# Performance work log

Measured on AMD Instinct MI355X. Metric: run time of the kernel, lower is better.

## Reference

```python
import jax, jax.numpy as jnp
import numpy as np

LAMBDA = 0.5
TAU = 1.0
EPS = 1e-8  # torch F.cosine_similarity eps

B, D = 8192, 1024


def setup_inputs() -> dict:
    key = jax.random.key(0)
    k1, k2, k3, k4 = jax.random.split(key, 4)
    return {
        "student_query_emb": jax.random.normal(k1, (B, D), dtype=jnp.float32),
        "student_passage_emb": jax.random.normal(k2, (B, D), dtype=jnp.float32),
        "teacher_query_emb": jax.random.normal(k3, (B, D), dtype=jnp.float32),
        "teacher_passage_emb": jax.random.normal(k4, (B, D), dtype=jnp.float32),
    }


def _mse(a, b):
    d = a - b
    return jnp.mean(d * d)


def _retrieval_loss(q, p):
    # cosine sim = (q . p) / max(||q|| * ||p||, eps); normalize then matmul
    # (avoids the [B,B,D] broadcast intermediate of the torch version)
    qn = q / jnp.maximum(jnp.linalg.norm(q, axis=-1, keepdims=True), EPS)
    pn = p / jnp.maximum(jnp.linalg.norm(p, axis=-1, keepdims=True), EPS)
    logits = jnp.einsum("bd,cd->bc", qn, pn) / TAU  # [B, B]
    # cross-entropy with labels = arange(B): pick the diagonal log-prob
    logprobs = jax.nn.log_softmax(logits, axis=-1)
    return -jnp.mean(jnp.diagonal(logprobs))


def reference(student_query_emb, student_passage_emb, teacher_query_emb, teacher_passage_emb):
    distill = 0.5 * (_mse(student_query_emb, teacher_query_emb)
                     + _mse(student_passage_emb, teacher_passage_emb))
    retrieval = _retrieval_loss(student_query_emb, student_passage_emb)
    return LAMBDA * distill + (1.0 - LAMBDA) * retrieval
```

## Files before the change

kernel.cpp:

```cpp
#include <hip/hip_runtime.h>
#include <hip/hip_bf16.h>

typedef unsigned short u16;
typedef unsigned char u8;
typedef float f32x4 __attribute__((ext_vector_type(4)));
typedef int int4v __attribute__((ext_vector_type(4)));
typedef int int8v __attribute__((ext_vector_type(8)));

#define B_ROWS 8192
#define D_DIM  1024
#define FP8_SCALE 16.0f
#define ACC_UNSCALE (1.0f/256.0f)


__global__ void __launch_bounds__(256) prep_kernel(
    const float* __restrict__ sq, const float* __restrict__ sp,
    const float* __restrict__ tq, const float* __restrict__ tp,
    int* __restrict__ qn, int* __restrict__ pn,
    float* __restrict__ ppq, float* __restrict__ ppp, float* __restrict__ ppd)
{
    const int wave = threadIdx.x >> 6;
    const int l    = threadIdx.x & 63;
    const int r    = blockIdx.x * 4 + wave;
    const size_t rb4 = (size_t)r * (D_DIM / 4);

    const float4* Q4 = (const float4*)sq + rb4;
    const float4* P4 = (const float4*)sp + rb4;
    const float4* A4 = (const float4*)tq + rb4;
    const float4* B4 = (const float4*)tp + rb4;

    float4 qv[4], pv[4];
    float sq2 = 0.f, sp2 = 0.f, dq = 0.f, dp = 0.f, qp = 0.f;
    #pragma unroll
    for (int j = 0; j < 4; ++j) {
        const int idx = j * 64 + l;
        float4 q = Q4[idx], p = P4[idx], a = A4[idx], b = B4[idx];
        qv[j] = q; pv[j] = p;
        sq2 += q.x*q.x + q.y*q.y + q.z*q.z + q.w*q.w;
        sp2 += p.x*p.x + p.y*p.y + p.z*p.z + p.w*p.w;
        float dx = q.x-a.x, dy = q.y-a.y, dz = q.z-a.z, dw = q.w-a.w;
        dq += dx*dx + dy*dy + dz*dz + dw*dw;
        dx = p.x-b.x; dy = p.y-b.y; dz = p.z-b.z; dw = p.w-b.w;
        dp += dx*dx + dy*dy + dz*dz + dw*dw;
        qp += q.x*p.x + q.y*p.y + q.z*p.z + q.w*p.w;
    }

    #pragma unroll
    for (int m = 1; m <= 32; m <<= 1) {
        sq2 += __shfl_xor(sq2, m);
        sp2 += __shfl_xor(sp2, m);
        dq  += __shfl_xor(dq, m);
        dp  += __shfl_xor(dp, m);
        qp  += __shfl_xor(qp, m);
    }

    const float rq = 1.0f / fmaxf(sqrtf(sq2), 1e-8f);
    const float rp = 1.0f / fmaxf(sqrtf(sp2), 1e-8f);

    if (l == 0) {
        ppq[r] = dq;
        ppp[r] = dp;
        ppd[r] = qp * rq * rp;
    }

    const float fq = rq * FP8_SCALE;
    const float fp = rp * FP8_SCALE;
    int* qrow = qn + (size_t)r * (D_DIM / 4);
    int* prow = pn + (size_t)r * (D_DIM / 4);
    #pragma unroll
    for (int j = 0; j < 4; ++j) {
        const int idx = j * 64 + l;
        int pk = __builtin_amdgcn_cvt_pk_fp8_f32(qv[j].x * fq, qv[j].y * fq, 0, false);
        pk     = __builtin_amdgcn_cvt_pk_fp8_f32(qv[j].z * fq, qv[j].w * fq, pk, true);
        qrow[idx] = pk;
        pk = __builtin_amdgcn_cvt_pk_fp8_f32(pv[j].x * fp, pv[j].y * fp, 0, false);
        pk = __builtin_amdgcn_cvt_pk_fp8_f32(pv[j].z * fp, pv[j].w * fp, pk, true);
        prow[idx] = pk;
    }
}

union Frag { int8v v8; struct { int4v lo, hi; } h; };

__global__ void __launch_bounds__(256, 3) gemm_rowsum_kernel(
    const u8* __restrict__ Q, const u8* __restrict__ P,
    float* __restrict__ gpart)
{
    __shared__ u8 smA[128 * 128];
    __shared__ u8 smB[128 * 128];

    const int tid  = threadIdx.x;
    const int wave = tid >> 6;
    const int lane = tid & 63;
    const int wm   = wave >> 1;
    const int wn   = wave & 1;
    const int bm   = blockIdx.y;
    const int bn   = blockIdx.x;

    const int srow   = tid >> 3;
    const int schunk = (tid & 7) ^ (srow & 7);
    const u8* Ag = Q + (size_t)(bm * 128 + srow) * D_DIM + schunk * 16;
    const u8* Bg = P + (size_t)(bn * 128 + srow) * D_DIM + schunk * 16;
    const int ldsw = wave * 1024;

#define STAGE_A(rbase, k0)                                                     \
    __builtin_amdgcn_global_load_lds(                                          \
        (const __attribute__((address_space(1))) void*)(Ag + (size_t)(rbase) * D_DIM + (k0)), \
        (__attribute__((address_space(3))) void*)(smA + (rbase) * 128 + ldsw), 16, 0, 0)
#define STAGE_B(rbase, k0)                                                     \
    __builtin_amdgcn_global_load_lds(                                          \
        (const __attribute__((address_space(1))) void*)(Bg + (size_t)(rbase) * D_DIM + (k0)), \
        (__attribute__((address_space(3))) void*)(smB + (rbase) * 128 + ldsw), 16, 0, 0)

#define STAGE_ALL(k0)                                                          \
    STAGE_A(0, k0); STAGE_A(32, k0); STAGE_A(64, k0); STAGE_A(96, k0);         \
    STAGE_B(0, k0); STAGE_B(32, k0); STAGE_B(64, k0); STAGE_B(96, k0);

    const int quad = lane >> 4;
    const int rw   = lane & 15;
    const int r7   = lane & 7;
    const int off_lo = ((2 * quad) ^ r7) * 16;
    const int off_hi = ((2 * quad + 1) ^ r7) * 16;
    const int arow_base = (wm * 64 + rw) * 128;
    const int brow_base = (wn * 64 + rw) * 128;

    f32x4 acc[4][4];
    #pragma unroll
    for (int i = 0; i < 4; ++i)
        #pragma unroll
        for (int j = 0; j < 4; ++j)
            acc[i][j] = (f32x4){0.f, 0.f, 0.f, 0.f};

    STAGE_ALL(0)

#define SB0 __builtin_amdgcn_sched_barrier(0);

#define MFMA1(mi, ni)                                                          \
    acc[mi][ni] = __builtin_amdgcn_mfma_scale_f32_16x16x128_f8f6f4(            \
        af[mi].v8, bf[ni].v8, acc[mi][ni],                                     \
        0, 0, 0, 0x7f7f7f7f, 0, 0x7f7f7f7f);

#define KSTEP(t, DO_NEXT)                                                      \
  {                                                                            \
    Frag af[4], bf[4];                                                         \
                           \
    asm volatile("s_waitcnt vmcnt(0)" ::: "memory");                           \
    __builtin_amdgcn_s_barrier();                                              \
    SB0                                                                        \
                                    \
    _Pragma("unroll")                                                          \
    for (int mi = 0; mi < 4; ++mi)                                             \
      af[mi].h.lo = *(const int4v*)(smA + arow_base + mi * 2048 + off_lo);     \
    _Pragma("unroll")                                                          \
    for (int ni = 0; ni < 4; ++ni)                                             \
      bf[ni].h.lo = *(const int4v*)(smB + brow_base + ni * 2048 + off_lo);     \
    SB0                                                                        \
    _Pragma("unroll")                                                          \
    for (int mi = 0; mi < 4; ++mi)                                             \
      af[mi].h.hi = *(const int4v*)(smA + arow_base + mi * 2048 + off_hi);     \
    _Pragma("unroll")                                                          \
    for (int ni = 0; ni < 4; ++ni)                                             \
      bf[ni].h.hi = *(const int4v*)(smB + brow_base + ni * 2048 + off_hi);     \
    asm volatile("s_waitcnt lgkmcnt(0)" ::: "memory");                         \
    SB0                                                                        \
    __builtin_amdgcn_s_barrier();      \
    SB0                                                                        \
            \
    if (DO_NEXT) { STAGE_ALL(((t) + 1) * 128) }                                \
    __builtin_amdgcn_s_setprio(1);                                             \
    MFMA1(0, 0) MFMA1(0, 1) MFMA1(1, 0) MFMA1(1, 1)                            \
    MFMA1(0, 2) MFMA1(0, 3) MFMA1(1, 2) MFMA1(1, 3)                            \
    MFMA1(2, 0) MFMA1(2, 1) MFMA1(3, 0) MFMA1(3, 1)                            \
    MFMA1(2, 2) MFMA1(2, 3) MFMA1(3, 2) MFMA1(3, 3)                            \
    __builtin_amdgcn_s_setprio(0);                                             \
  }

    KSTEP(0, true)
    KSTEP(1, true)
    KSTEP(2, true)
    KSTEP(3, true)
    KSTEP(4, true)
    KSTEP(5, true)
    KSTEP(6, true)
    KSTEP(7, false)

#undef KSTEP
#undef MFMA1
#undef SB0
#undef STAGE_ALL
#undef STAGE_A
#undef STAGE_B

    float esum[4][4];
    #pragma unroll
    for (int mi = 0; mi < 4; ++mi)
        #pragma unroll
        for (int r = 0; r < 4; ++r) {
            float s = 0.f;
            #pragma unroll
            for (int ni = 0; ni < 4; ++ni)
                s += __expf(acc[mi][ni][r] * ACC_UNSCALE);
            esum[mi][r] = s;
        }
    #pragma unroll
    for (int m = 1; m <= 8; m <<= 1)
        #pragma unroll
        for (int mi = 0; mi < 4; ++mi)
            #pragma unroll
            for (int r = 0; r < 4; ++r)
                esum[mi][r] += __shfl_xor(esum[mi][r], m);

    if (rw == 0) {
        float* dst = gpart + (size_t)(bn * 2 + wn) * B_ROWS
                   + bm * 128 + wm * 64;
        #pragma unroll
        for (int mi = 0; mi < 4; ++mi)
            #pragma unroll
            for (int r = 0; r < 4; ++r)
                dst[mi * 16 + quad * 4 + r] = esum[mi][r];
    }
}

__global__ void __launch_bounds__(256) reduce_kernel(
    const float* __restrict__ gpart,
    const float* __restrict__ ppq, const float* __restrict__ ppp,
    const float* __restrict__ ppd, float4* __restrict__ bpart)
{
    const int t = threadIdx.x;
    const int r = blockIdx.x * 256 + t;
    float s = 0.f;
    #pragma unroll 8
    for (int j = 0; j < 128; ++j) s += gpart[(size_t)j * B_ROWS + r];
    float ls = logf(s);
    float v2 = ppq[r], v3 = ppp[r], v4 = ppd[r];
    #pragma unroll
    for (int m = 1; m <= 32; m <<= 1) {
        ls += __shfl_xor(ls, m);
        v2 += __shfl_xor(v2, m);
        v3 += __shfl_xor(v3, m);
        v4 += __shfl_xor(v4, m);
    }
    __shared__ float red[4][4];
    if ((t & 63) == 0) {
        red[t >> 6][0] = ls; red[t >> 6][1] = v2;
        red[t >> 6][2] = v3; red[t >> 6][3] = v4;
    }
    __syncthreads();
    if (t == 0) {
        float4 o;
        o.x = red[0][0] + red[1][0] + red[2][0] + red[3][0];
        o.y = red[0][1] + red[1][1] + red[2][1] + red[3][1];
        o.z = red[0][2] + red[1][2] + red[2][2] + red[3][2];
        o.w = red[0][3] + red[1][3] + red[2][3] + red[3][3];
        bpart[blockIdx.x] = o;
    }
}

__global__ void __launch_bounds__(64) finalize_kernel(
    const float4* __restrict__ bpart, float* __restrict__ out)
{
    const int t = threadIdx.x;
    float4 v = (t < 32) ? bpart[t] : (float4){0.f, 0.f, 0.f, 0.f};
    #pragma unroll
    for (int m = 1; m <= 16; m <<= 1) {
        v.x += __shfl_xor(v.x, m);
        v.y += __shfl_xor(v.y, m);
        v.z += __shfl_xor(v.z, m);
        v.w += __shfl_xor(v.w, m);
    }
    if (t == 0) {
        const float inv_bd = 1.0f / ((float)B_ROWS * (float)D_DIM);
        float distill   = 0.5f * (v.y + v.z) * inv_bd;
        float retrieval = (v.x - v.w) / (float)B_ROWS;
        out[0] = 0.5f * distill + 0.5f * retrieval;
    }
}

extern "C" void kernel_launch(void* const* d_in, const int* in_sizes, int n_in,
                              void* d_out, int out_size, void* d_ws, size_t ws_size,
                              hipStream_t stream) {
    const float* sq = (const float*)d_in[0];
    const float* sp = (const float*)d_in[1];
    const float* tq = (const float*)d_in[2];
    const float* tp = (const float*)d_in[3];

    char* ws = (char*)d_ws;
    float*  ppq   = (float*)(ws);
    float*  ppp   = (float*)(ws + 32768);
    float*  ppd   = (float*)(ws + 65536);
    float4* bpart = (float4*)(ws + 98304);
    float*  gpart = (float*)(ws + 131072);
    int*    qn    = (int*)(ws + 131072 + (size_t)128 * B_ROWS * 4);
    int*    pn    = (int*)((char*)qn + (size_t)B_ROWS * D_DIM);

    prep_kernel<<<B_ROWS / 4, 256, 0, stream>>>(sq, sp, tq, tp, qn, pn, ppq, ppp, ppd);
    gemm_rowsum_kernel<<<dim3(64, 64), 256, 0, stream>>>((const u8*)qn, (const u8*)pn, gpart);
    reduce_kernel<<<32, 256, 0, stream>>>(gpart, ppq, ppp, ppd, bpart);
    finalize_kernel<<<1, 64, 0, stream>>>(bpart, (float*)d_out);
}
```

Baseline: 232.0 us.

## Load B operand fragments directly from global memory, bypassing LDS staging

The P (B-operand) tile is no longer staged through shared memory. Each lane now reads its MFMA B fragments straight from global memory into registers, and the vmcnt waits are reworked so these loads overlap the A-tile LDS staging. This halves LDS usage and the LDS read traffic, which can raise occupancy and cut barrier-bound LDS traffic. The cost is that B data is no longer shared between the two waves that use the same columns, so global and L2 traffic for P roughly doubles. The per-lane 16-byte loads are also strided by rows, which may coalesce poorly.

```diff
diff --git a/kernel.cpp b/kernel.cpp
--- a/kernel.cpp
+++ b/kernel.cpp
@@ -86,7 +86,6 @@
     float* __restrict__ gpart)
 {
     __shared__ u8 smA[128 * 128];
-    __shared__ u8 smB[128 * 128];
 
     const int tid  = threadIdx.x;
     const int wave = tid >> 6;
@@ -99,21 +98,15 @@
     const int srow   = tid >> 3;
     const int schunk = (tid & 7) ^ (srow & 7);
     const u8* Ag = Q + (size_t)(bm * 128 + srow) * D_DIM + schunk * 16;
-    const u8* Bg = P + (size_t)(bn * 128 + srow) * D_DIM + schunk * 16;
     const int ldsw = wave * 1024;
 
 #define STAGE_A(rbase, k0)                                                     \
     __builtin_amdgcn_global_load_lds(                                          \
         (const __attribute__((address_space(1))) void*)(Ag + (size_t)(rbase) * D_DIM + (k0)), \
         (__attribute__((address_space(3))) void*)(smA + (rbase) * 128 + ldsw), 16, 0, 0)
-#define STAGE_B(rbase, k0)                                                     \
-    __builtin_amdgcn_global_load_lds(                                          \
-        (const __attribute__((address_space(1))) void*)(Bg + (size_t)(rbase) * D_DIM + (k0)), \
-        (__attribute__((address_space(3))) void*)(smB + (rbase) * 128 + ldsw), 16, 0, 0)
 
 #define STAGE_ALL(k0)                                                          \
-    STAGE_A(0, k0); STAGE_A(32, k0); STAGE_A(64, k0); STAGE_A(96, k0);         \
-    STAGE_B(0, k0); STAGE_B(32, k0); STAGE_B(64, k0); STAGE_B(96, k0);
+    STAGE_A(0, k0); STAGE_A(32, k0); STAGE_A(64, k0); STAGE_A(96, k0);
 
     const int quad = lane >> 4;
     const int rw   = lane & 15;
@@ -121,7 +114,8 @@
     const int off_lo = ((2 * quad) ^ r7) * 16;
     const int off_hi = ((2 * quad + 1) ^ r7) * 16;
     const int arow_base = (wm * 64 + rw) * 128;
-    const int brow_base = (wn * 64 + rw) * 128;
+
+    const u8* Bd = P + (size_t)(bn * 128 + wn * 64 + rw) * D_DIM + quad * 32;
 
     f32x4 acc[4][4];
     #pragma unroll
@@ -139,33 +133,35 @@
         af[mi].v8, bf[ni].v8, acc[mi][ni],                                     \
         0, 0, 0, 0x7f7f7f7f, 0, 0x7f7f7f7f);
 
-#define KSTEP(t, DO_NEXT)                                                      \
+#define KSTEP(t, DO_NEXT, VMN)                                                 \
   {                                                                            \
     Frag af[4], bf[4];                                                         \
-                           \
-    asm volatile("s_waitcnt vmcnt(0)" ::: "memory");                           \
+         \
+    _Pragma("unroll")                                                          \
+    for (int ni = 0; ni < 4; ++ni) {                                           \
+      bf[ni].h.lo = *(const int4v*)(Bd + (size_t)ni * 16 * D_DIM + (t) * 128);        \
+      bf[ni].h.hi = *(const int4v*)(Bd + (size_t)ni * 16 * D_DIM + (t) * 128 + 16);   \
+    }                                                                          \
+                       \
+    asm volatile("s_waitcnt vmcnt(8)" ::: "memory");                           \
     __builtin_amdgcn_s_barrier();                                              \
     SB0                                                                        \
-                                    \
+                                   \
     _Pragma("unroll")                                                          \
     for (int mi = 0; mi < 4; ++mi)                                             \
       af[mi].h.lo = *(const int4v*)(smA + arow_base + mi * 2048 + off_lo);     \
-    _Pragma("unroll")                                                          \
-    for (int ni = 0; ni < 4; ++ni)                                             \
-      bf[ni].h.lo = *(const int4v*)(smB + brow_base + ni * 2048 + off_lo);     \
     SB0                                                                        \
     _Pragma("unroll")                                                          \
     for (int mi = 0; mi < 4; ++mi)                                             \
       af[mi].h.hi = *(const int4v*)(smA + arow_base + mi * 2048 + off_hi);     \
-    _Pragma("unroll")                                                          \
-    for (int ni = 0; ni < 4; ++ni)                                             \
-      bf[ni].h.hi = *(const int4v*)(smB + brow_base + ni * 2048 + off_hi);     \
     asm volatile("s_waitcnt lgkmcnt(0)" ::: "memory");                         \
     SB0                                                                        \
     __builtin_amdgcn_s_barrier();      \
     SB0                                                                        \
-            \
+                   \
     if (DO_NEXT) { STAGE_ALL(((t) + 1) * 128) }                                \
+    asm volatile("s_waitcnt vmcnt(" #VMN ")" ::: "memory");                    \
+    SB0                                                                        \
     __builtin_amdgcn_s_setprio(1);                                             \
     MFMA1(0, 0) MFMA1(0, 1) MFMA1(1, 0) MFMA1(1, 1)                            \
     MFMA1(0, 2) MFMA1(0, 3) MFMA1(1, 2) MFMA1(1, 3)                            \
@@ -174,21 +170,20 @@
     __builtin_amdgcn_s_setprio(0);                                             \
   }
 
-    KSTEP(0, true)
-    KSTEP(1, true)
-    KSTEP(2, true)
-    KSTEP(3, true)
-    KSTEP(4, true)
-    KSTEP(5, true)
-    KSTEP(6, true)
-    KSTEP(7, false)
+    KSTEP(0, true,  4)
+    KSTEP(1, true,  4)
+    KSTEP(2, true,  4)
+    KSTEP(3, true,  4)
+    KSTEP(4, true,  4)
+    KSTEP(5, true,  4)
+    KSTEP(6, true,  4)
+    KSTEP(7, false, 0)
 
 #undef KSTEP
 #undef MFMA1
 #undef SB0
 #undef STAGE_ALL
 #undef STAGE_A
-#undef STAGE_B
 
     float esum[4][4];
     #pragma unroll
```

After: 294.9 us. 1.27x slower.
